# Kernel tuning notes

Measured on AMD Instinct MI355X. Metric: run time of the kernel, lower is better.

Reference implementation:

```python
import jax, jax.numpy as jnp
import numpy as np

B, C, T, H, Wd = 8, 256, 16, 28, 28

def setup_inputs() -> dict:
    key = jax.random.key(0)
    k1, k2 = jax.random.split(key)
    in_data = jax.random.normal(k1, (B, C, T, H, Wd), dtype=jnp.float32)
    # conv_whh weight [C, C, 1, 1, 1] squeezed to [C_out, C_in]; scaled like kaiming init
    W = jax.random.normal(k2, (C, C), dtype=jnp.float32) * (1.0 / jnp.sqrt(jnp.float32(C)))
    return {"in_data": in_data, "W": W}

def reference(in_data, W):
    # h_0 = x_0; h_t = (W @ h_{t-1} + x_t) / 2, out = stack over t
    x0 = in_data[:, :, 0]                      # [B, C, H, W]
    xs = jnp.moveaxis(in_data[:, :, 1:], 2, 0) # [T-1, B, C, H, W]

    def step(h, x_t):
        h_new = (jnp.einsum('oc,bchw->bohw', W, h) + x_t) * 0.5
        return h_new, h_new

    _, outs = jax.lax.scan(step, x0, xs)       # [T-1, B, C, H, W]
    out = jnp.concatenate([x0[None], outs], axis=0)  # [T, B, C, H, W]
    return jnp.moveaxis(out, 0, 2)             # [B, C, T, H, W]
```

## Files before the change

### kernel.cpp

```cpp
#include <hip/hip_runtime.h>


typedef __attribute__((ext_vector_type(8))) short bf16x8;
typedef __attribute__((ext_vector_type(4))) float f32x4;
typedef __attribute__((ext_vector_type(4))) short short4v;

#define NTILES 49
#define LDSK   264

#define LDS_BARRIER()                                                          \
    do {                                                                       \
        asm volatile("s_waitcnt lgkmcnt(0)" ::: "memory");                     \
        __builtin_amdgcn_s_barrier();                                          \
        __builtin_amdgcn_sched_barrier(0);                                     \
    } while (0)

__device__ __forceinline__ short f2bf(float f) {
    union { float f; unsigned u; } v; v.f = f;
    unsigned r = v.u + 0x7FFFu + ((v.u >> 16) & 1u);
    return (short)(r >> 16);
}

__global__ __launch_bounds__(256, 2)
void rcu_kernel(const float* __restrict__ in, const float* __restrict__ Wm,
                float* __restrict__ out) {
    __shared__ short hbuf[2][16][LDSK];

    const int tid  = threadIdx.x;
    const int wave = tid >> 6;
    const int lane = tid & 63;
    const int l15  = lane & 15;
    const int quad = lane >> 4;

    const int b  = blockIdx.x / NTILES;
    const int s0 = (blockIdx.x % NTILES) * 16;

    const size_t base = (size_t)b * 256 * 16 * 784 + s0;
    const float* xin  = in  + base;
    float*       xout = out + base;

    bf16x8 a_frag[4][8];
#pragma unroll
    for (int mt = 0; mt < 4; ++mt) {
        const int m = wave * 64 + mt * 16 + l15;
        const float* wrow = Wm + m * 256 + quad * 8;
#pragma unroll
        for (int ks = 0; ks < 8; ++ks) {
            float4 f0 = *(const float4*)(wrow + ks * 32);
            float4 f1 = *(const float4*)(wrow + ks * 32 + 4);
            bf16x8 a;
            a[0] = f2bf(f0.x); a[1] = f2bf(f0.y); a[2] = f2bf(f0.z); a[3] = f2bf(f0.w);
            a[4] = f2bf(f1.x); a[5] = f2bf(f1.y); a[6] = f2bf(f1.z); a[7] = f2bf(f1.w);
            a_frag[mt][ks] = a;
        }
    }

    {
        const int sg = tid & 15;
        const int cg = tid >> 4;
#pragma unroll
        for (int i = 0; i < 16; ++i) {
            const int c = cg * 16 + i;
            const size_t off = (size_t)c * 12544 + sg;
            const float v = xin[off];
            xout[off] = v;
            hbuf[0][sg][c] = f2bf(v);
        }
    }

    float xr[2][16];

#pragma unroll
    for (int mt = 0; mt < 4; ++mt)
#pragma unroll
        for (int r = 0; r < 4; ++r) {
            const int c = wave * 64 + mt * 16 + quad * 4 + r;
            xr[1][mt * 4 + r] = xin[((size_t)c * 16 + 1) * 784 + l15];
        }

    LDS_BARRIER();

    int cur = 0;
#pragma unroll
    for (int t = 1; t < 16; ++t) {
        const int xb = t & 1;

        if (t < 15) {
#pragma unroll
            for (int mt = 0; mt < 4; ++mt)
#pragma unroll
                for (int r = 0; r < 4; ++r) {
                    const int c = wave * 64 + mt * 16 + quad * 4 + r;
                    xr[xb ^ 1][mt * 4 + r] =
                        xin[((size_t)c * 16 + t + 1) * 784 + l15];
                }
        }

        bf16x8 bfrag[8];
        const short* hp = &hbuf[cur][l15][quad * 8];
#pragma unroll
        for (int ks = 0; ks < 8; ++ks)
            bfrag[ks] = *(const bf16x8*)(hp + ks * 32);

        f32x4 acc[4];
#pragma unroll
        for (int mt = 0; mt < 4; ++mt) {
            acc[mt] = (f32x4){0.f, 0.f, 0.f, 0.f};
#pragma unroll
            for (int ks = 0; ks < 8; ++ks)
                acc[mt] = __builtin_amdgcn_mfma_f32_16x16x32_bf16(
                    a_frag[mt][ks], bfrag[ks], acc[mt], 0, 0, 0);
        }

        const int nxt = cur ^ 1;
#pragma unroll
        for (int mt = 0; mt < 4; ++mt) {
            const int c0 = wave * 64 + mt * 16 + quad * 4;
            short4v hbf;
#pragma unroll
            for (int r = 0; r < 4; ++r) {
                const float v = 0.5f * (acc[mt][r] + xr[xb][mt * 4 + r]);
                xout[((size_t)(c0 + r) * 16 + t) * 784 + l15] = v;
                hbf[r] = f2bf(v);
            }
            *(short4v*)&hbuf[nxt][l15][c0] = hbf;
        }
        LDS_BARRIER();
        cur = nxt;
    }
}

extern "C" void kernel_launch(void* const* d_in, const int* in_sizes, int n_in,
                              void* d_out, int out_size, void* d_ws, size_t ws_size,
                              hipStream_t stream) {
    const float* in  = (const float*)d_in[0];
    const float* Wm  = (const float*)d_in[1];
    float*       out = (float*)d_out;
    hipLaunchKernelGGL(rcu_kernel, dim3(8 * NTILES), dim3(256), 0, stream, in, Wm, out);
}
```

Baseline: 229.5 us.

## Widen spatial tile to 32 and split output channels across 8 waves

Each block now covers 32 spatial positions with 512 threads, and each of the 8 waves owns 32 output channels and two 16-wide spatial subtiles. The last tile per batch takes a 16-wide path through a templated helper. The intent is to halve the per-wave weight fragments and the register pressure while keeping the same MFMA work per wave per step, and to halve the block count. The cost is that only 200 blocks are launched, fewer than the CU count, so some CUs sit idle. Every block also synchronizes twice as many waves at each timestep barrier.

```diff
diff --git a/kernel.cpp b/kernel.cpp
--- a/kernel.cpp
+++ b/kernel.cpp
@@ -5,8 +5,8 @@
 typedef __attribute__((ext_vector_type(4))) float f32x4;
 typedef __attribute__((ext_vector_type(4))) short short4v;
 
-#define NTILES 49
-#define LDSK   264
+#define TILES_PER_B 25
+#define LDSK 264
 
 #define LDS_BARRIER()                                                          \
     do {                                                                       \
@@ -21,28 +21,21 @@
     return (short)(r >> 16);
 }
 
-__global__ __launch_bounds__(256, 2)
-void rcu_kernel(const float* __restrict__ in, const float* __restrict__ Wm,
-                float* __restrict__ out) {
-    __shared__ short hbuf[2][16][LDSK];
-
+template <int NT>
+__device__ __forceinline__ void run_tile(const float* __restrict__ xin,
+                                         float* __restrict__ xout,
+                                         const float* __restrict__ Wm,
+                                         short (*hbuf)[32][LDSK]) {
     const int tid  = threadIdx.x;
     const int wave = tid >> 6;
     const int lane = tid & 63;
     const int l15  = lane & 15;
     const int quad = lane >> 4;
 
-    const int b  = blockIdx.x / NTILES;
-    const int s0 = (blockIdx.x % NTILES) * 16;
-
-    const size_t base = (size_t)b * 256 * 16 * 784 + s0;
-    const float* xin  = in  + base;
-    float*       xout = out + base;
-
-    bf16x8 a_frag[4][8];
+    bf16x8 a_frag[2][8];
 #pragma unroll
-    for (int mt = 0; mt < 4; ++mt) {
-        const int m = wave * 64 + mt * 16 + l15;
+    for (int mt = 0; mt < 2; ++mt) {
+        const int m = wave * 32 + mt * 16 + l15;
         const float* wrow = Wm + m * 256 + quad * 8;
 #pragma unroll
         for (int ks = 0; ks < 8; ++ks) {
@@ -56,11 +49,13 @@
     }
 
     {
-        const int sg = tid & 15;
-        const int cg = tid >> 4;
+        const int NS  = 16 * NT;
+        const int sg  = tid & (NS - 1);
+        const int cg  = tid / NS;
+        const int CPT = NS / 2;
 #pragma unroll
-        for (int i = 0; i < 16; ++i) {
-            const int c = cg * 16 + i;
+        for (int i = 0; i < CPT; ++i) {
+            const int c = cg * CPT + i;
             const size_t off = (size_t)c * 12544 + sg;
             const float v = xin[off];
             xout[off] = v;
@@ -68,15 +63,17 @@
         }
     }
 
-    float xr[2][16];
+    float xr[2][2][NT][4];
 
 #pragma unroll
-    for (int mt = 0; mt < 4; ++mt)
+    for (int mt = 0; mt < 2; ++mt)
 #pragma unroll
-        for (int r = 0; r < 4; ++r) {
-            const int c = wave * 64 + mt * 16 + quad * 4 + r;
-            xr[1][mt * 4 + r] = xin[((size_t)c * 16 + 1) * 784 + l15];
-        }
+        for (int nt = 0; nt < NT; ++nt)
+#pragma unroll
+            for (int r = 0; r < 4; ++r) {
+                const int c = wave * 32 + mt * 16 + quad * 4 + r;
+                xr[1][mt][nt][r] = xin[((size_t)c * 16 + 1) * 784 + nt * 16 + l15];
+            }
 
     LDS_BARRIER();
 
@@ -87,47 +84,70 @@
 
         if (t < 15) {
 #pragma unroll
-            for (int mt = 0; mt < 4; ++mt)
+            for (int mt = 0; mt < 2; ++mt)
 #pragma unroll
-                for (int r = 0; r < 4; ++r) {
-                    const int c = wave * 64 + mt * 16 + quad * 4 + r;
-                    xr[xb ^ 1][mt * 4 + r] =
-                        xin[((size_t)c * 16 + t + 1) * 784 + l15];
-                }
+                for (int nt = 0; nt < NT; ++nt)
+#pragma unroll
+                    for (int r = 0; r < 4; ++r) {
+                        const int c = wave * 32 + mt * 16 + quad * 4 + r;
+                        xr[xb ^ 1][mt][nt][r] =
+                            xin[((size_t)c * 16 + t + 1) * 784 + nt * 16 + l15];
+                    }
         }
 
-        bf16x8 bfrag[8];
-        const short* hp = &hbuf[cur][l15][quad * 8];
+        bf16x8 bfrag[NT][8];
 #pragma unroll
-        for (int ks = 0; ks < 8; ++ks)
-            bfrag[ks] = *(const bf16x8*)(hp + ks * 32);
-
-        f32x4 acc[4];
-#pragma unroll
-        for (int mt = 0; mt < 4; ++mt) {
-            acc[mt] = (f32x4){0.f, 0.f, 0.f, 0.f};
+        for (int nt = 0; nt < NT; ++nt) {
+            const short* hp = &hbuf[cur][nt * 16 + l15][quad * 8];
 #pragma unroll
             for (int ks = 0; ks < 8; ++ks)
-                acc[mt] = __builtin_amdgcn_mfma_f32_16x16x32_bf16(
-                    a_frag[mt][ks], bfrag[ks], acc[mt], 0, 0, 0);
+                bfrag[nt][ks] = *(const bf16x8*)(hp + ks * 32);
         }
+
+        f32x4 acc[2][NT];
+#pragma unroll
+        for (int mt = 0; mt < 2; ++mt)
+#pragma unroll
+            for (int nt = 0; nt < NT; ++nt) {
+                acc[mt][nt] = (f32x4){0.f, 0.f, 0.f, 0.f};
+#pragma unroll
+                for (int ks = 0; ks < 8; ++ks)
+                    acc[mt][nt] = __builtin_amdgcn_mfma_f32_16x16x32_bf16(
+                        a_frag[mt][ks], bfrag[nt][ks], acc[mt][nt], 0, 0, 0);
+            }
 
         const int nxt = cur ^ 1;
 #pragma unroll
-        for (int mt = 0; mt < 4; ++mt) {
-            const int c0 = wave * 64 + mt * 16 + quad * 4;
-            short4v hbf;
+        for (int mt = 0; mt < 2; ++mt) {
+            const int c0 = wave * 32 + mt * 16 + quad * 4;
 #pragma unroll
-            for (int r = 0; r < 4; ++r) {
-                const float v = 0.5f * (acc[mt][r] + xr[xb][mt * 4 + r]);
-                xout[((size_t)(c0 + r) * 16 + t) * 784 + l15] = v;
-                hbf[r] = f2bf(v);
+            for (int nt = 0; nt < NT; ++nt) {
+                short4v hbf;
+#pragma unroll
+                for (int r = 0; r < 4; ++r) {
+                    const float v = 0.5f * (acc[mt][nt][r] + xr[xb][mt][nt][r]);
+                    xout[((size_t)(c0 + r) * 16 + t) * 784 + nt * 16 + l15] = v;
+                    hbf[r] = f2bf(v);
+                }
+                *(short4v*)&hbuf[nxt][nt * 16 + l15][c0] = hbf;
             }
-            *(short4v*)&hbuf[nxt][l15][c0] = hbf;
         }
         LDS_BARRIER();
         cur = nxt;
     }
+}
+
+__global__ __launch_bounds__(512, 2)
+void rcu_kernel(const float* __restrict__ in, const float* __restrict__ Wm,
+                float* __restrict__ out) {
+    __shared__ short hbuf[2][32][LDSK];
+
+    const int b = blockIdx.x / TILES_PER_B;
+    const int j = blockIdx.x % TILES_PER_B;
+    const size_t base = (size_t)b * 256 * 16 * 784 + (size_t)j * 32;
+
+    if (j < 24) run_tile<2>(in + base, out + base, Wm, hbuf);
+    else        run_tile<1>(in + base, out + base, Wm, hbuf);
 }
 
 extern "C" void kernel_launch(void* const* d_in, const int* in_sizes, int n_in,
@@ -136,5 +156,6 @@
     const float* in  = (const float*)d_in[0];
     const float* Wm  = (const float*)d_in[1];
     float*       out = (float*)d_out;
-    hipLaunchKernelGGL(rcu_kernel, dim3(8 * NTILES), dim3(256), 0, stream, in, Wm, out);
+    hipLaunchKernelGGL(rcu_kernel, dim3(8 * TILES_PER_B), dim3(512), 0, stream,
+                       in, Wm, out);
 }
```

New measurement: 209.5 us. 8.7% less time.
